# Optimization experiments

Hardware: AMD Instinct MI355X
Metric: run time of the kernel (lower is better)

The kernel has to match this reference:

```python
import jax, jax.numpy as jnp
import numpy as np

M = 3          # num_modes
B = 64         # batch
D = 512        # feat_dim
HIST = 5       # history_len (deque pre-filled with HIST zero matrices)
SMOOTH = 0.8   # smooth_factor


def setup_inputs() -> dict:
    ks = jax.random.split(jax.random.key(0), 6)
    return {
        "x": jax.random.normal(ks[0], (M, B, D), jnp.float32),
        "proj_W": jax.random.normal(ks[1], (M, D, D), jnp.float32) * 0.02,
        "proj_b": jnp.zeros((M, D), jnp.float32),
        "ln_g": jnp.ones((M, D), jnp.float32),
        "ln_b": jnp.zeros((M, D), jnp.float32),
        "imp_W1": jax.random.normal(ks[2], (M, D // 4, D), jnp.float32) * 0.02,
        "imp_b1": jnp.zeros((M, D // 4), jnp.float32),
        "imp_W2": jax.random.normal(ks[3], (M, D, D // 4), jnp.float32) * 0.02,
        "imp_b2": jnp.zeros((M, D), jnp.float32),
        "gamma": jax.random.normal(ks[4], (M, M), jnp.float32) * 0.1,
        "modal_bias": jax.random.normal(ks[5], (M, M), jnp.float32) * 0.01,
        "constraint": jnp.ones((M,), jnp.float32) * 0.2,
    }


def _layernorm(v, g, b, eps=1e-5):
    mu = v.mean(-1, keepdims=True)
    var = ((v - mu) ** 2).mean(-1, keepdims=True)
    return (v - mu) / jnp.sqrt(var + eps) * g + b


def reference(x, proj_W, proj_b, ln_g, ln_b, imp_W1, imp_b1, imp_W2, imp_b2,
              gamma, modal_bias, constraint):
    scale = D ** 0.5
    # per-mode projector: Linear -> LayerNorm -> ReLU
    proj = [jax.nn.relu(_layernorm(x[i] @ proj_W[i].T + proj_b[i], ln_g[i], ln_b[i]))
            for i in range(M)]
    # channel importance: Linear -> ReLU -> Linear -> Sigmoid
    cw = [jax.nn.sigmoid(
              jax.nn.relu(proj[i] @ imp_W1[i].T + imp_b1[i]) @ imp_W2[i].T + imp_b2[i])
          for i in range(M)]
    wf = [proj[i] * cw[i] for i in range(M)]  # weighted features [B, D]

    interactions, scores = [], []
    for i in range(M):
        # deque holds HIST zero matrices; appends within this forward replace
        # zeros, so the running mean is sum(appended)/HIST.
        hist_sum = jnp.zeros((D, D), x.dtype)
        hist = hist_sum / HIST
        c = constraint[i]
        feats, gs = [], []
        for j in range(M):
            if i == j:
                continue
            cur = jnp.einsum('bd,be->bde', wf[i], wf[j]) / scale  # [B, D, D]
            constrained = hist + jnp.clip(cur - hist, -c, c)
            final = SMOOTH * constrained + (1.0 - SMOOTH) * cur
            # append detached batch-mean to history
            hist_sum = hist_sum + jax.lax.stop_gradient(final.mean(0))
            hist = hist_sum / HIST
            attn = jax.nn.softmax(final, axis=-1) + modal_bias[i, j]
            g = jax.nn.sigmoid(gamma[i, j])
            attended = jnp.einsum('bde,be->bd', attn, wf[j])  # bmm(attn, value)
            feats.append(g * attended + wf[i])
            gs.append(g)
        interactions.append(jnp.stack(feats).mean(0))
        scores.append(jnp.stack(gs).mean())
    fused = jnp.stack(interactions).mean(0)              # [B, D]
    attention_weights = jax.nn.softmax(jnp.stack(scores))  # [M]
    return fused, attention_weights
```

## Files before the change

kernel.cpp:

```cpp
#include <hip/hip_runtime.h>
#include <math.h>

#define M_ 3
#define B_ 64
#define D_ 512
#define H4 128
#define HIST_ 5
#define BD (B_ * D_)
#define INVSCALE 0.04419417382415922f
#define LOG2E 1.4426950408889634f

__device__ __forceinline__ float wave_sum64(float v) {
#pragma unroll
    for (int o = 32; o >= 1; o >>= 1) v += __shfl_xor(v, o, 64);
    return v;
}

__device__ __forceinline__ float sigmoidf(float x) {
    return 1.0f / (1.0f + __expf(-x));
}

__global__ __launch_bounds__(512) void k_proj(
    const float* __restrict__ x, const float* __restrict__ pW,
    float* __restrict__ ypart)
{
    const int m  = blockIdx.x >> 7;
    const int rem = blockIdx.x & 127;
    const int b0 = (rem >> 2) << 1;
    const int kq = rem & 3;
    const int t  = threadIdx.x;

    __shared__ __align__(16) float4 xs[2][32];
    if (t < 64) {
        const int r = t >> 5, c = t & 31;
        xs[r][c] = ((const float4*)(x + (size_t)(m * B_ + b0 + r) * D_ + kq * 128))[c];
    }
    __syncthreads();

    const float4* wr = (const float4*)(pW + (size_t)m * D_ * D_ + (size_t)t * D_ + kq * 128);
    float acc0 = 0.f, acc1 = 0.f;
#pragma unroll
    for (int k = 0; k < 32; ++k) {
        const float4 w = wr[k];
        const float4 a = xs[0][k];
        const float4 b = xs[1][k];
        acc0 = fmaf(w.x, a.x, acc0); acc0 = fmaf(w.y, a.y, acc0);
        acc0 = fmaf(w.z, a.z, acc0); acc0 = fmaf(w.w, a.w, acc0);
        acc1 = fmaf(w.x, b.x, acc1); acc1 = fmaf(w.y, b.y, acc1);
        acc1 = fmaf(w.z, b.z, acc1); acc1 = fmaf(w.w, b.w, acc1);
    }
    const size_t idx0 = (size_t)(m * B_ + b0) * 2048 + kq * 512 + t;
    ypart[idx0]        = acc0;
    ypart[idx0 + 2048] = acc1;
}

__global__ __launch_bounds__(512) void k_lnmlp(
    const float* __restrict__ ypart, const float* __restrict__ pb,
    const float* __restrict__ lg, const float* __restrict__ lb,
    const float* __restrict__ W1, const float* __restrict__ b1,
    const float* __restrict__ W2, const float* __restrict__ b2,
    float* __restrict__ wf, float* __restrict__ Ssum)
{
    const int m = blockIdx.x >> 6;
    const int b = blockIdx.x & 63;
    const int t = threadIdx.x;
    __shared__ __align__(16) float ps[D_];
    __shared__ __align__(16) float hs[H4];
    __shared__ __align__(16) float hpart[512];
    __shared__ float red[8];

    const size_t rbase = (size_t)(m * B_ + b) * 2048;
    const float y = ypart[rbase + t] + ypart[rbase + 512 + t]
                  + ypart[rbase + 1024 + t] + ypart[rbase + 1536 + t]
                  + pb[m * D_ + t];

    float s = wave_sum64(y);
    if ((t & 63) == 0) red[t >> 6] = s;
    __syncthreads();
    const float mean = (red[0]+red[1]+red[2]+red[3]+red[4]+red[5]+red[6]+red[7]) * (1.f / D_);
    __syncthreads();
    const float v = y - mean;
    float vs = wave_sum64(v * v);
    if ((t & 63) == 0) red[t >> 6] = vs;
    __syncthreads();
    const float inv = rsqrtf((red[0]+red[1]+red[2]+red[3]+red[4]+red[5]+red[6]+red[7]) * (1.f / D_) + 1e-5f);
    const float p = fmaxf(fmaf(v * inv, lg[m * D_ + t], lb[m * D_ + t]), 0.f);
    ps[t] = p;
    __syncthreads();

    {
        const int r = t & 127, seg = t >> 7;
        const float4* w1 = (const float4*)(W1 + ((size_t)m * H4 + r) * D_) + (seg << 5);
        const float4* pv = (const float4*)ps + (seg << 5);
        float a1 = 0.f;
#pragma unroll
        for (int k = 0; k < 32; ++k) {
            const float4 w = w1[k], pp = pv[k];
            a1 = fmaf(w.x, pp.x, a1); a1 = fmaf(w.y, pp.y, a1);
            a1 = fmaf(w.z, pp.z, a1); a1 = fmaf(w.w, pp.w, a1);
        }
        hpart[t] = a1;
    }
    __syncthreads();
    if (t < H4)
        hs[t] = fmaxf(hpart[t] + hpart[t + 128] + hpart[t + 256] + hpart[t + 384]
                      + b1[m * H4 + t], 0.f);
    __syncthreads();

    const float4* w2 = (const float4*)(W2 + ((size_t)m * D_ + t) * H4);
    const float4* hv = (const float4*)hs;
    float a2 = 0.f;
#pragma unroll
    for (int k = 0; k < H4 / 4; ++k) {
        const float4 w = w2[k], hh = hv[k];
        a2 = fmaf(w.x, hh.x, a2); a2 = fmaf(w.y, hh.y, a2);
        a2 = fmaf(w.z, hh.z, a2); a2 = fmaf(w.w, hh.w, a2);
    }
    const float cw = sigmoidf(a2 + b2[m * D_ + t]);
    const float wv = p * cw;
    wf[(size_t)(m * B_ + b) * D_ + t] = wv;

    float tot = wave_sum64(wv);
    if ((t & 63) == 0) red[t >> 6] = tot;
    __syncthreads();
    if (t == 0)
        Ssum[m * B_ + b] = red[0]+red[1]+red[2]+red[3]+red[4]+red[5]+red[6]+red[7];
}

__global__ __launch_bounds__(256) void k_hist(
    const float* __restrict__ wf, const float* __restrict__ constraint,
    float* __restrict__ HT)
{
    const int i  = blockIdx.x >> 8;
    const int e0 = (blockIdx.x & 255) << 1;
    const int j  = (i == 0) ? 1 : 0;
    const int t  = threadIdx.x;
    const float c = constraint[i];
    const float* wfi = wf + (size_t)i * BD;
    const float* wfj = wf + (size_t)j * BD;

    float h00 = 0.f, h01 = 0.f, h10 = 0.f, h11 = 0.f;
    for (int b = 0; b < B_; ++b) {
        const float a0 = wfi[b * D_ + t]       * INVSCALE;
        const float a1 = wfi[b * D_ + t + 256] * INVSCALE;
        const float2 u2 = *(const float2*)(wfj + b * D_ + e0);
        float tt, mm;
        tt = a0 * u2.x; mm = fminf(fmaxf(tt, -c), c); h00 = fmaf(0.8f, mm, fmaf(0.2f, tt, h00));
        tt = a1 * u2.x; mm = fminf(fmaxf(tt, -c), c); h01 = fmaf(0.8f, mm, fmaf(0.2f, tt, h01));
        tt = a0 * u2.y; mm = fminf(fmaxf(tt, -c), c); h10 = fmaf(0.8f, mm, fmaf(0.2f, tt, h10));
        tt = a1 * u2.y; mm = fminf(fmaxf(tt, -c), c); h11 = fmaf(0.8f, mm, fmaf(0.2f, tt, h11));
    }
    const float hsc = LOG2E / (float)(B_ * HIST_);
    float* r0 = HT + ((size_t)(i << 9) + e0) * D_;
    r0[t]             = h00 * hsc;
    r0[t + 256]       = h01 * hsc;
    r0[D_ + t]        = h10 * hsc;
    r0[D_ + t + 256]  = h11 * hsc;
}

__global__ __launch_bounds__(256) void k_passAB(
    const float* __restrict__ wf, const float* __restrict__ constraint,
    const float* __restrict__ gamma, const float* __restrict__ mbias,
    const float* __restrict__ HT, const float* __restrict__ Ssum,
    float* __restrict__ pair)
{
    const int i    = blockIdx.x >> 9;
    const int rem  = blockIdx.x & 511;
    const int b    = rem >> 3;
    const int dc   = rem & 7;
    const int t    = threadIdx.x;
    const int d    = (dc << 6) + (t & 63);
    const int esec = t >> 6;
    const int jA = (i == 0) ? 1 : 0;
    const int jB = (i == 2) ? 1 : 2;

    const float cl = constraint[i] * LOG2E;
    const float a  = wf[(size_t)i * BD + b * D_ + d] * (INVSCALE * LOG2E);
    const float* uAp = wf + (size_t)jA * BD + b * D_ + (esec << 7);
    const float* uBp = wf + (size_t)jB * BD + b * D_ + (esec << 7);
    const float* Hp  = HT + ((size_t)(i << 9) + (esec << 7)) * D_ + d;

    float sA = 0.f, dA = 0.f;
#pragma unroll 4
    for (int e = 0; e < 128; e += 4) {
        const float4 u4 = *(const float4*)(uAp + e);
        const float uu[4] = {u4.x, u4.y, u4.z, u4.w};
#pragma unroll
        for (int k = 0; k < 4; ++k) {
            const float tt = a * uu[k];
            const float mm = fminf(fmaxf(tt, -cl), cl);
            const float f  = fmaf(0.8f, mm, 0.2f * tt);
            const float p  = __builtin_amdgcn_exp2f(f);
            sA += p;
            dA = fmaf(p, uu[k], dA);
        }
    }

    float sB = 0.f, dB = 0.f;
    const float* hp = Hp;
#pragma unroll 2
    for (int e = 0; e < 128; e += 4) {
        const float4 u4 = *(const float4*)(uBp + e);
        const float uu[4] = {u4.x, u4.y, u4.z, u4.w};
        float hh[4];
#pragma unroll
        for (int k = 0; k < 4; ++k) hh[k] = hp[(size_t)k * D_];
        hp += 4 * D_;
#pragma unroll
        for (int k = 0; k < 4; ++k) {
            const float tt = a * uu[k];
            const float df = tt - hh[k];
            const float mm = fminf(fmaxf(df, -cl), cl);
            const float f  = fmaf(0.8f, hh[k] + mm, 0.2f * tt);
            const float p  = __builtin_amdgcn_exp2f(f);
            sB += p;
            dB = fmaf(p, uu[k], dB);
        }
    }

    __shared__ __align__(16) float4 part[256];
    part[t] = make_float4(sA, dA, sB, dB);
    __syncthreads();
    if (t < 64) {
        const float4 p0 = part[t], p1 = part[t + 64], p2 = part[t + 128], p3 = part[t + 192];
        const float SsA = p0.x + p1.x + p2.x + p3.x;
        const float SdA = p0.y + p1.y + p2.y + p3.y;
        const float SsB = p0.z + p1.z + p2.z + p3.z;
        const float SdB = p0.w + p1.w + p2.w + p3.w;
        const float gA = sigmoidf(gamma[i * 3 + jA]);
        const float gB = sigmoidf(gamma[i * 3 + jB]);
        const float pv = gA * (SdA / SsA + mbias[i * 3 + jA] * Ssum[jA * B_ + b])
                       + gB * (SdB / SsB + mbias[i * 3 + jB] * Ssum[jB * B_ + b]);
        pair[(size_t)i * BD + b * D_ + d] = pv;
    }
}

__global__ __launch_bounds__(256) void k_combine(
    const float* __restrict__ wf, const float* __restrict__ pair,
    const float* __restrict__ gamma, float* __restrict__ out)
{
    const int g = blockIdx.x * 256 + threadIdx.x;
    const float w0 = wf[g], w1 = wf[BD + g], w2 = wf[2 * BD + g];
    const float p0 = pair[g], p1 = pair[BD + g], p2 = pair[2 * BD + g];
    out[g] = fmaf(p0 + p1 + p2, 1.f / 6.f, (w0 + w1 + w2) * (1.f / 3.f));

    if (g == 0) {
        const float g01 = sigmoidf(gamma[1]), g02 = sigmoidf(gamma[2]);
        const float g10 = sigmoidf(gamma[3]), g12 = sigmoidf(gamma[5]);
        const float g20 = sigmoidf(gamma[6]), g21 = sigmoidf(gamma[7]);
        const float s0 = 0.5f * (g01 + g02);
        const float s1 = 0.5f * (g10 + g12);
        const float s2 = 0.5f * (g20 + g21);
        const float mx = fmaxf(s0, fmaxf(s1, s2));
        const float e0 = __expf(s0 - mx), e1 = __expf(s1 - mx), e2 = __expf(s2 - mx);
        const float den = e0 + e1 + e2;
        out[BD + 0] = e0 / den;
        out[BD + 1] = e1 / den;
        out[BD + 2] = e2 / den;
    }
}

extern "C" void kernel_launch(void* const* d_in, const int* in_sizes, int n_in,
                              void* d_out, int out_size, void* d_ws, size_t ws_size,
                              hipStream_t stream) {
    const float* x    = (const float*)d_in[0];
    const float* pW   = (const float*)d_in[1];
    const float* pb   = (const float*)d_in[2];
    const float* lg   = (const float*)d_in[3];
    const float* lb   = (const float*)d_in[4];
    const float* W1   = (const float*)d_in[5];
    const float* b1   = (const float*)d_in[6];
    const float* W2   = (const float*)d_in[7];
    const float* b2   = (const float*)d_in[8];
    const float* gamma= (const float*)d_in[9];
    const float* mb   = (const float*)d_in[10];
    const float* cons = (const float*)d_in[11];
    float* out = (float*)d_out;

    float* ws    = (float*)d_ws;
    float* wf    = ws;
    float* Ssum  = ws + 98304;
    float* HT    = ws + 98496;
    float* ypart = ws + 884928;
    float* pair  = ypart;

    k_proj   <<<dim3(384),      dim3(512), 0, stream>>>(x, pW, ypart);
    k_lnmlp  <<<dim3(M_ * B_),  dim3(512), 0, stream>>>(ypart, pb, lg, lb, W1, b1, W2, b2, wf, Ssum);
    k_hist   <<<dim3(M_ * 256), dim3(256), 0, stream>>>(wf, cons, HT);
    k_passAB <<<dim3(M_ * 512), dim3(256), 0, stream>>>(wf, cons, gamma, mb, HT, Ssum, pair);
    k_combine<<<dim3(128),      dim3(256), 0, stream>>>(wf, pair, gamma, out);
}
```

Baseline: 161.8 us.

## Drop combine kernel via atomic accumulation and retile proj/passAB grids

Removes the final combine kernel: lnmlp and passAB now atomically add their scaled contributions straight into the output, which is zeroed by a memset, and the attention-weight softmax moves into k_proj. k_proj is split into twice as many 256-thread blocks, passAB is split into twice as many blocks with shorter inner loops and an 8-way reduction, and k_hist gets unroll hints. The goal is less launch overhead, no pair buffer round-trip, and more parallelism. In exchange it adds a memset launch, atomic contention on the output, and a floating-point summation order that is no longer deterministic.

```diff
diff --git a/kernel.cpp b/kernel.cpp
--- a/kernel.cpp
+++ b/kernel.cpp
@@ -20,24 +20,29 @@
     return 1.0f / (1.0f + __expf(-x));
 }
 
-__global__ __launch_bounds__(512) void k_proj(
+__global__ __launch_bounds__(256) void k_proj(
     const float* __restrict__ x, const float* __restrict__ pW,
-    float* __restrict__ ypart)
-{
-    const int m  = blockIdx.x >> 7;
-    const int rem = blockIdx.x & 127;
-    const int b0 = (rem >> 2) << 1;
-    const int kq = rem & 3;
-    const int t  = threadIdx.x;
+    const float* __restrict__ gamma, float* __restrict__ ypart,
+    float* __restrict__ out)
+{
+    const int m    = blockIdx.x >> 8;
+    const int r    = blockIdx.x & 255;
+    const int kq   = r >> 6;
+    const int rem2 = r & 63;
+    const int dh   = rem2 >> 5;
+    const int bp   = rem2 & 31;
+    const int b0   = bp << 1;
+    const int t    = threadIdx.x;
+    const int d    = (dh << 8) + t;
 
     __shared__ __align__(16) float4 xs[2][32];
     if (t < 64) {
-        const int r = t >> 5, c = t & 31;
-        xs[r][c] = ((const float4*)(x + (size_t)(m * B_ + b0 + r) * D_ + kq * 128))[c];
-    }
-    __syncthreads();
-
-    const float4* wr = (const float4*)(pW + (size_t)m * D_ * D_ + (size_t)t * D_ + kq * 128);
+        const int rr = t >> 5, cc = t & 31;
+        xs[rr][cc] = ((const float4*)(x + (size_t)(m * B_ + b0 + rr) * D_ + kq * 128))[cc];
+    }
+    __syncthreads();
+
+    const float4* wr = (const float4*)(pW + (size_t)m * D_ * D_ + (size_t)d * D_ + kq * 128);
     float acc0 = 0.f, acc1 = 0.f;
 #pragma unroll
     for (int k = 0; k < 32; ++k) {
@@ -49,202 +54,11 @@
         acc1 = fmaf(w.x, b.x, acc1); acc1 = fmaf(w.y, b.y, acc1);
         acc1 = fmaf(w.z, b.z, acc1); acc1 = fmaf(w.w, b.w, acc1);
     }
-    const size_t idx0 = (size_t)(m * B_ + b0) * 2048 + kq * 512 + t;
+    const size_t idx0 = (size_t)(m * B_ + b0) * 2048 + kq * 512 + d;
     ypart[idx0]        = acc0;
     ypart[idx0 + 2048] = acc1;
-}
-
-__global__ __launch_bounds__(512) void k_lnmlp(
-    const float* __restrict__ ypart, const float* __restrict__ pb,
-    const float* __restrict__ lg, const float* __restrict__ lb,
-    const float* __restrict__ W1, const float* __restrict__ b1,
-    const float* __restrict__ W2, const float* __restrict__ b2,
-    float* __restrict__ wf, float* __restrict__ Ssum)
-{
-    const int m = blockIdx.x >> 6;
-    const int b = blockIdx.x & 63;
-    const int t = threadIdx.x;
-    __shared__ __align__(16) float ps[D_];
-    __shared__ __align__(16) float hs[H4];
-    __shared__ __align__(16) float hpart[512];
-    __shared__ float red[8];
-
-    const size_t rbase = (size_t)(m * B_ + b) * 2048;
-    const float y = ypart[rbase + t] + ypart[rbase + 512 + t]
-                  + ypart[rbase + 1024 + t] + ypart[rbase + 1536 + t]
-                  + pb[m * D_ + t];
-
-    float s = wave_sum64(y);
-    if ((t & 63) == 0) red[t >> 6] = s;
-    __syncthreads();
-    const float mean = (red[0]+red[1]+red[2]+red[3]+red[4]+red[5]+red[6]+red[7]) * (1.f / D_);
-    __syncthreads();
-    const float v = y - mean;
-    float vs = wave_sum64(v * v);
-    if ((t & 63) == 0) red[t >> 6] = vs;
-    __syncthreads();
-    const float inv = rsqrtf((red[0]+red[1]+red[2]+red[3]+red[4]+red[5]+red[6]+red[7]) * (1.f / D_) + 1e-5f);
-    const float p = fmaxf(fmaf(v * inv, lg[m * D_ + t], lb[m * D_ + t]), 0.f);
-    ps[t] = p;
-    __syncthreads();
-
-    {
-        const int r = t & 127, seg = t >> 7;
-        const float4* w1 = (const float4*)(W1 + ((size_t)m * H4 + r) * D_) + (seg << 5);
-        const float4* pv = (const float4*)ps + (seg << 5);
-        float a1 = 0.f;
-#pragma unroll
-        for (int k = 0; k < 32; ++k) {
-            const float4 w = w1[k], pp = pv[k];
-            a1 = fmaf(w.x, pp.x, a1); a1 = fmaf(w.y, pp.y, a1);
-            a1 = fmaf(w.z, pp.z, a1); a1 = fmaf(w.w, pp.w, a1);
-        }
-        hpart[t] = a1;
-    }
-    __syncthreads();
-    if (t < H4)
-        hs[t] = fmaxf(hpart[t] + hpart[t + 128] + hpart[t + 256] + hpart[t + 384]
-                      + b1[m * H4 + t], 0.f);
-    __syncthreads();
-
-    const float4* w2 = (const float4*)(W2 + ((size_t)m * D_ + t) * H4);
-    const float4* hv = (const float4*)hs;
-    float a2 = 0.f;
-#pragma unroll
-    for (int k = 0; k < H4 / 4; ++k) {
-        const float4 w = w2[k], hh = hv[k];
-        a2 = fmaf(w.x, hh.x, a2); a2 = fmaf(w.y, hh.y, a2);
-        a2 = fmaf(w.z, hh.z, a2); a2 = fmaf(w.w, hh.w, a2);
-    }
-    const float cw = sigmoidf(a2 + b2[m * D_ + t]);
-    const float wv = p * cw;
-    wf[(size_t)(m * B_ + b) * D_ + t] = wv;
-
-    float tot = wave_sum64(wv);
-    if ((t & 63) == 0) red[t >> 6] = tot;
-    __syncthreads();
-    if (t == 0)
-        Ssum[m * B_ + b] = red[0]+red[1]+red[2]+red[3]+red[4]+red[5]+red[6]+red[7];
-}
-
-__global__ __launch_bounds__(256) void k_hist(
-    const float* __restrict__ wf, const float* __restrict__ constraint,
-    float* __restrict__ HT)
-{
-    const int i  = blockIdx.x >> 8;
-    const int e0 = (blockIdx.x & 255) << 1;
-    const int j  = (i == 0) ? 1 : 0;
-    const int t  = threadIdx.x;
-    const float c = constraint[i];
-    const float* wfi = wf + (size_t)i * BD;
-    const float* wfj = wf + (size_t)j * BD;
-
-    float h00 = 0.f, h01 = 0.f, h10 = 0.f, h11 = 0.f;
-    for (int b = 0; b < B_; ++b) {
-        const float a0 = wfi[b * D_ + t]       * INVSCALE;
-        const float a1 = wfi[b * D_ + t + 256] * INVSCALE;
-        const float2 u2 = *(const float2*)(wfj + b * D_ + e0);
-        float tt, mm;
-        tt = a0 * u2.x; mm = fminf(fmaxf(tt, -c), c); h00 = fmaf(0.8f, mm, fmaf(0.2f, tt, h00));
-        tt = a1 * u2.x; mm = fminf(fmaxf(tt, -c), c); h01 = fmaf(0.8f, mm, fmaf(0.2f, tt, h01));
-        tt = a0 * u2.y; mm = fminf(fmaxf(tt, -c), c); h10 = fmaf(0.8f, mm, fmaf(0.2f, tt, h10));
-        tt = a1 * u2.y; mm = fminf(fmaxf(tt, -c), c); h11 = fmaf(0.8f, mm, fmaf(0.2f, tt, h11));
-    }
-    const float hsc = LOG2E / (float)(B_ * HIST_);
-    float* r0 = HT + ((size_t)(i << 9) + e0) * D_;
-    r0[t]             = h00 * hsc;
-    r0[t + 256]       = h01 * hsc;
-    r0[D_ + t]        = h10 * hsc;
-    r0[D_ + t + 256]  = h11 * hsc;
-}
-
-__global__ __launch_bounds__(256) void k_passAB(
-    const float* __restrict__ wf, const float* __restrict__ constraint,
-    const float* __restrict__ gamma, const float* __restrict__ mbias,
-    const float* __restrict__ HT, const float* __restrict__ Ssum,
-    float* __restrict__ pair)
-{
-    const int i    = blockIdx.x >> 9;
-    const int rem  = blockIdx.x & 511;
-    const int b    = rem >> 3;
-    const int dc   = rem & 7;
-    const int t    = threadIdx.x;
-    const int d    = (dc << 6) + (t & 63);
-    const int esec = t >> 6;
-    const int jA = (i == 0) ? 1 : 0;
-    const int jB = (i == 2) ? 1 : 2;
-
-    const float cl = constraint[i] * LOG2E;
-    const float a  = wf[(size_t)i * BD + b * D_ + d] * (INVSCALE * LOG2E);
-    const float* uAp = wf + (size_t)jA * BD + b * D_ + (esec << 7);
-    const float* uBp = wf + (size_t)jB * BD + b * D_ + (esec << 7);
-    const float* Hp  = HT + ((size_t)(i << 9) + (esec << 7)) * D_ + d;
-
-    float sA = 0.f, dA = 0.f;
-#pragma unroll 4
-    for (int e = 0; e < 128; e += 4) {
-        const float4 u4 = *(const float4*)(uAp + e);
-        const float uu[4] = {u4.x, u4.y, u4.z, u4.w};
-#pragma unroll
-        for (int k = 0; k < 4; ++k) {
-            const float tt = a * uu[k];
-            const float mm = fminf(fmaxf(tt, -cl), cl);
-            const float f  = fmaf(0.8f, mm, 0.2f * tt);
-            const float p  = __builtin_amdgcn_exp2f(f);
-            sA += p;
-            dA = fmaf(p, uu[k], dA);
-        }
-    }
-
-    float sB = 0.f, dB = 0.f;
-    const float* hp = Hp;
-#pragma unroll 2
-    for (int e = 0; e < 128; e += 4) {
-        const float4 u4 = *(const float4*)(uBp + e);
-        const float uu[4] = {u4.x, u4.y, u4.z, u4.w};
-        float hh[4];
-#pragma unroll
-        for (int k = 0; k < 4; ++k) hh[k] = hp[(size_t)k * D_];
-        hp += 4 * D_;
-#pragma unroll
-        for (int k = 0; k < 4; ++k) {
-            const float tt = a * uu[k];
-            const float df = tt - hh[k];
-            const float mm = fminf(fmaxf(df, -cl), cl);
-            const float f  = fmaf(0.8f, hh[k] + mm, 0.2f * tt);
-            const float p  = __builtin_amdgcn_exp2f(f);
-            sB += p;
-            dB = fmaf(p, uu[k], dB);
-        }
-    }
-
-    __shared__ __align__(16) float4 part[256];
-    part[t] = make_float4(sA, dA, sB, dB);
-    __syncthreads();
-    if (t < 64) {
-        const float4 p0 = part[t], p1 = part[t + 64], p2 = part[t + 128], p3 = part[t + 192];
-        const float SsA = p0.x + p1.x + p2.x + p3.x;
-        const float SdA = p0.y + p1.y + p2.y + p3.y;
-        const float SsB = p0.z + p1.z + p2.z + p3.z;
-        const float SdB = p0.w + p1.w + p2.w + p3.w;
-        const float gA = sigmoidf(gamma[i * 3 + jA]);
-        const float gB = sigmoidf(gamma[i * 3 + jB]);
-        const float pv = gA * (SdA / SsA + mbias[i * 3 + jA] * Ssum[jA * B_ + b])
-                       + gB * (SdB / SsB + mbias[i * 3 + jB] * Ssum[jB * B_ + b]);
-        pair[(size_t)i * BD + b * D_ + d] = pv;
-    }
-}
-
-__global__ __launch_bounds__(256) void k_combine(
-    const float* __restrict__ wf, const float* __restrict__ pair,
-    const float* __restrict__ gamma, float* __restrict__ out)
-{
-    const int g = blockIdx.x * 256 + threadIdx.x;
-    const float w0 = wf[g], w1 = wf[BD + g], w2 = wf[2 * BD + g];
-    const float p0 = pair[g], p1 = pair[BD + g], p2 = pair[2 * BD + g];
-    out[g] = fmaf(p0 + p1 + p2, 1.f / 6.f, (w0 + w1 + w2) * (1.f / 3.f));
-
-    if (g == 0) {
+
+    if (blockIdx.x == 0 && t == 0) {
         const float g01 = sigmoidf(gamma[1]), g02 = sigmoidf(gamma[2]);
         const float g10 = sigmoidf(gamma[3]), g12 = sigmoidf(gamma[5]);
         const float g20 = sigmoidf(gamma[6]), g21 = sigmoidf(gamma[7]);
@@ -257,6 +71,191 @@
         out[BD + 0] = e0 / den;
         out[BD + 1] = e1 / den;
         out[BD + 2] = e2 / den;
+    }
+}
+
+__global__ __launch_bounds__(512) void k_lnmlp(
+    const float* __restrict__ ypart, const float* __restrict__ pb,
+    const float* __restrict__ lg, const float* __restrict__ lb,
+    const float* __restrict__ W1, const float* __restrict__ b1,
+    const float* __restrict__ W2, const float* __restrict__ b2,
+    float* __restrict__ wf, float* __restrict__ Ssum,
+    float* __restrict__ out)
+{
+    const int m = blockIdx.x >> 6;
+    const int b = blockIdx.x & 63;
+    const int t = threadIdx.x;
+    __shared__ __align__(16) float ps[D_];
+    __shared__ __align__(16) float hs[H4];
+    __shared__ __align__(16) float hpart[512];
+    __shared__ float red[8];
+
+    const size_t rbase = (size_t)(m * B_ + b) * 2048;
+    const float y = ypart[rbase + t] + ypart[rbase + 512 + t]
+                  + ypart[rbase + 1024 + t] + ypart[rbase + 1536 + t]
+                  + pb[m * D_ + t];
+
+    float s = wave_sum64(y);
+    if ((t & 63) == 0) red[t >> 6] = s;
+    __syncthreads();
+    const float mean = (red[0]+red[1]+red[2]+red[3]+red[4]+red[5]+red[6]+red[7]) * (1.f / D_);
+    __syncthreads();
+    const float v = y - mean;
+    float vs = wave_sum64(v * v);
+    if ((t & 63) == 0) red[t >> 6] = vs;
+    __syncthreads();
+    const float inv = rsqrtf((red[0]+red[1]+red[2]+red[3]+red[4]+red[5]+red[6]+red[7]) * (1.f / D_) + 1e-5f);
+    const float p = fmaxf(fmaf(v * inv, lg[m * D_ + t], lb[m * D_ + t]), 0.f);
+    ps[t] = p;
+    __syncthreads();
+
+    {
+        const int r = t & 127, seg = t >> 7;
+        const float4* w1 = (const float4*)(W1 + ((size_t)m * H4 + r) * D_) + (seg << 5);
+        const float4* pv = (const float4*)ps + (seg << 5);
+        float a1 = 0.f;
+#pragma unroll
+        for (int k = 0; k < 32; ++k) {
+            const float4 w = w1[k], pp = pv[k];
+            a1 = fmaf(w.x, pp.x, a1); a1 = fmaf(w.y, pp.y, a1);
+            a1 = fmaf(w.z, pp.z, a1); a1 = fmaf(w.w, pp.w, a1);
+        }
+        hpart[t] = a1;
+    }
+    __syncthreads();
+    if (t < H4)
+        hs[t] = fmaxf(hpart[t] + hpart[t + 128] + hpart[t + 256] + hpart[t + 384]
+                      + b1[m * H4 + t], 0.f);
+    __syncthreads();
+
+    const float4* w2 = (const float4*)(W2 + ((size_t)m * D_ + t) * H4);
+    const float4* hv = (const float4*)hs;
+    float a2 = 0.f;
+#pragma unroll
+    for (int k = 0; k < H4 / 4; ++k) {
+        const float4 w = w2[k], hh = hv[k];
+        a2 = fmaf(w.x, hh.x, a2); a2 = fmaf(w.y, hh.y, a2);
+        a2 = fmaf(w.z, hh.z, a2); a2 = fmaf(w.w, hh.w, a2);
+    }
+    const float cw = sigmoidf(a2 + b2[m * D_ + t]);
+    const float wv = p * cw;
+    wf[(size_t)(m * B_ + b) * D_ + t] = wv;
+    atomicAdd(&out[b * D_ + t], wv * (1.f / 3.f));
+
+    float tot = wave_sum64(wv);
+    if ((t & 63) == 0) red[t >> 6] = tot;
+    __syncthreads();
+    if (t == 0)
+        Ssum[m * B_ + b] = red[0]+red[1]+red[2]+red[3]+red[4]+red[5]+red[6]+red[7];
+}
+
+__global__ __launch_bounds__(256) void k_hist(
+    const float* __restrict__ wf, const float* __restrict__ constraint,
+    float* __restrict__ HT)
+{
+    const int i  = blockIdx.x >> 8;
+    const int e0 = (blockIdx.x & 255) << 1;
+    const int j  = (i == 0) ? 1 : 0;
+    const int t  = threadIdx.x;
+    const float c = constraint[i];
+    const float* wfi = wf + (size_t)i * BD;
+    const float* wfj = wf + (size_t)j * BD;
+
+    float h00 = 0.f, h01 = 0.f, h10 = 0.f, h11 = 0.f;
+#pragma unroll 4
+    for (int b = 0; b < B_; ++b) {
+        const float a0 = wfi[b * D_ + t]       * INVSCALE;
+        const float a1 = wfi[b * D_ + t + 256] * INVSCALE;
+        const float2 u2 = *(const float2*)(wfj + b * D_ + e0);
+        float tt, mm;
+        tt = a0 * u2.x; mm = fminf(fmaxf(tt, -c), c); h00 = fmaf(0.8f, mm, fmaf(0.2f, tt, h00));
+        tt = a1 * u2.x; mm = fminf(fmaxf(tt, -c), c); h01 = fmaf(0.8f, mm, fmaf(0.2f, tt, h01));
+        tt = a0 * u2.y; mm = fminf(fmaxf(tt, -c), c); h10 = fmaf(0.8f, mm, fmaf(0.2f, tt, h10));
+        tt = a1 * u2.y; mm = fminf(fmaxf(tt, -c), c); h11 = fmaf(0.8f, mm, fmaf(0.2f, tt, h11));
+    }
+    const float hsc = LOG2E / (float)(B_ * HIST_);
+    float* r0 = HT + ((size_t)(i << 9) + e0) * D_;
+    r0[t]             = h00 * hsc;
+    r0[t + 256]       = h01 * hsc;
+    r0[D_ + t]        = h10 * hsc;
+    r0[D_ + t + 256]  = h11 * hsc;
+}
+
+__global__ __launch_bounds__(256) void k_passAB(
+    const float* __restrict__ wf, const float* __restrict__ constraint,
+    const float* __restrict__ gamma, const float* __restrict__ mbias,
+    const float* __restrict__ HT, const float* __restrict__ Ssum,
+    float* __restrict__ out)
+{
+    const int i    = blockIdx.x >> 10;
+    const int rem  = blockIdx.x & 1023;
+    const int b    = rem >> 4;
+    const int dc   = rem & 15;
+    const int t    = threadIdx.x;
+    const int d    = (dc << 5) + (t & 31);
+    const int esec = t >> 5;
+    const int jA = (i == 0) ? 1 : 0;
+    const int jB = (i == 2) ? 1 : 2;
+
+    const float cl = constraint[i] * LOG2E;
+    const float a  = wf[(size_t)i * BD + b * D_ + d] * (INVSCALE * LOG2E);
+    const float* uAp = wf + (size_t)jA * BD + b * D_ + (esec << 6);
+    const float* uBp = wf + (size_t)jB * BD + b * D_ + (esec << 6);
+    const float* Hp  = HT + ((size_t)(i << 9) + (esec << 6)) * D_ + d;
+
+    float sA = 0.f, dA = 0.f;
+#pragma unroll 4
+    for (int e = 0; e < 64; e += 4) {
+        const float4 u4 = *(const float4*)(uAp + e);
+        const float uu[4] = {u4.x, u4.y, u4.z, u4.w};
+#pragma unroll
+        for (int k = 0; k < 4; ++k) {
+            const float tt = a * uu[k];
+            const float mm = fminf(fmaxf(tt, -cl), cl);
+            const float f  = fmaf(0.8f, mm, 0.2f * tt);
+            const float p  = __builtin_amdgcn_exp2f(f);
+            sA += p;
+            dA = fmaf(p, uu[k], dA);
+        }
+    }
+
+    float sB = 0.f, dB = 0.f;
+    const float* hp = Hp;
+#pragma unroll 4
+    for (int e = 0; e < 64; e += 4) {
+        const float4 u4 = *(const float4*)(uBp + e);
+        const float uu[4] = {u4.x, u4.y, u4.z, u4.w};
+        float hh[4];
+#pragma unroll
+        for (int k = 0; k < 4; ++k) hh[k] = hp[(size_t)k * D_];
+        hp += 4 * D_;
+#pragma unroll
+        for (int k = 0; k < 4; ++k) {
+            const float tt = a * uu[k];
+            const float df = tt - hh[k];
+            const float mm = fminf(fmaxf(df, -cl), cl);
+            const float f  = fmaf(0.8f, hh[k] + mm, 0.2f * tt);
+            const float p  = __builtin_amdgcn_exp2f(f);
+            sB += p;
+            dB = fmaf(p, uu[k], dB);
+        }
+    }
+
+    __shared__ __align__(16) float4 part[256];
+    part[t] = make_float4(sA, dA, sB, dB);
+    __syncthreads();
+    if (t < 32) {
+        float SsA = 0.f, SdA = 0.f, SsB = 0.f, SdB = 0.f;
+#pragma unroll
+        for (int k = 0; k < 8; ++k) {
+            const float4 pp = part[t + (k << 5)];
+            SsA += pp.x; SdA += pp.y; SsB += pp.z; SdB += pp.w;
+        }
+        const float gA = sigmoidf(gamma[i * 3 + jA]);
+        const float gB = sigmoidf(gamma[i * 3 + jB]);
+        const float pv = gA * (SdA / SsA + mbias[i * 3 + jA] * Ssum[jA * B_ + b])
+                       + gB * (SdB / SsB + mbias[i * 3 + jB] * Ssum[jB * B_ + b]);
+        atomicAdd(&out[b * D_ + d], pv * (1.f / 6.f));
     }
 }
 
@@ -282,11 +281,11 @@
     float* Ssum  = ws + 98304;
     float* HT    = ws + 98496;
     float* ypart = ws + 884928;
-    float* pair  = ypart;
-
-    k_proj   <<<dim3(384),      dim3(512), 0, stream>>>(x, pW, ypart);
-    k_lnmlp  <<<dim3(M_ * B_),  dim3(512), 0, stream>>>(ypart, pb, lg, lb, W1, b1, W2, b2, wf, Ssum);
-    k_hist   <<<dim3(M_ * 256), dim3(256), 0, stream>>>(wf, cons, HT);
-    k_passAB <<<dim3(M_ * 512), dim3(256), 0, stream>>>(wf, cons, gamma, mb, HT, Ssum, pair);
-    k_combine<<<dim3(128),      dim3(256), 0, stream>>>(wf, pair, gamma, out);
-}
+
+    hipMemsetAsync(out, 0, (size_t)BD * sizeof(float), stream);
+
+    k_proj  <<<dim3(768),       dim3(256), 0, stream>>>(x, pW, gamma, ypart, out);
+    k_lnmlp <<<dim3(M_ * B_),   dim3(512), 0, stream>>>(ypart, pb, lg, lb, W1, b1, W2, b2, wf, Ssum, out);
+    k_hist  <<<dim3(M_ * 256),  dim3(256), 0, stream>>>(wf, cons, HT);
+    k_passAB<<<dim3(M_ * 1024), dim3(256), 0, stream>>>(wf, cons, gamma, mb, HT, Ssum, out);
+}
```

Result: faster. 155.0 us (-4.2%).
